# Kernel tuning notes

Measured on AMD Instinct MI355X. Metric: run time of the kernel, lower is better.

The kernel has to match this reference:

```python
import jax, jax.numpy as jnp
import numpy as np

B, S, D, H = 2, 2048, 1024, 16
DH = D // H

def setup_inputs() -> dict:
    key = jax.random.key(0)
    k1, k2, k3, k4 = jax.random.split(key, 4)
    x = jax.random.normal(k1, (B, S, D), dtype=jnp.float32)
    # flax Dense kernels: [in_features, out_features]
    w_qkv = jax.random.normal(k2, (D, 3 * D), dtype=jnp.float32) / np.sqrt(D)
    w_out = jax.random.normal(k3, (D, D), dtype=jnp.float32) / np.sqrt(D)
    b_out = jax.random.normal(k4, (D,), dtype=jnp.float32) * 0.01
    return {"x": x, "w_qkv": w_qkv, "w_out": w_out, "b_out": b_out}

def reference(x, w_qkv, w_out, b_out):
    b, s, d = x.shape
    h, dh = H, d // H
    qkv = jnp.einsum('bsd,de->bse', x, w_qkv)           # [B,S,3D]
    qkv = qkv.reshape(b, s, 3, h, dh)
    qkv = jnp.transpose(qkv, (2, 0, 3, 1, 4))            # [3,B,H,S,DH]
    q, k, v = qkv[0], qkv[1], qkv[2]
    attn = jnp.einsum('bhqd,bhkd->bhqk', q, k) / jnp.sqrt(jnp.float32(dh))
    attn = jax.nn.softmax(attn, axis=-1)                 # [B,H,S,S]
    y = jnp.einsum('bhqk,bhkd->bhqd', attn, v)           # [B,H,S,DH]
    y = jnp.transpose(y, (0, 2, 1, 3)).reshape(b, s, d)  # [B,S,D]
    return jnp.einsum('bsd,de->bse', y, w_out) + b_out
```

## Files before the change

kernel.cpp:

```cpp
#include <hip/hip_runtime.h>
#include <stdint.h>

typedef __bf16 bf16_t;
typedef __bf16 bf16x8 __attribute__((ext_vector_type(8)));
typedef float f32x4 __attribute__((ext_vector_type(4)));
typedef float f32x16 __attribute__((ext_vector_type(16)));
typedef unsigned short u16;
typedef unsigned short u16x8 __attribute__((ext_vector_type(8)));
typedef unsigned int u32;
typedef unsigned int u32x4 __attribute__((ext_vector_type(4)));

#define DEVI __device__ __forceinline__


DEVI u16 bits(float f) { bf16_t h = (bf16_t)f; return __builtin_bit_cast(u16, h); }

DEVI void gld16(const void* g, void* l) {
  __builtin_amdgcn_global_load_lds(
      (const __attribute__((address_space(1))) unsigned int*)g,
      (__attribute__((address_space(3))) unsigned int*)l, 16, 0, 0);
}

DEVI bf16x8 ldsr(const u16* s, int row, int cg) {
  const int byte = row * 128 + ((cg ^ (row & 7)) << 4);
  return *(const bf16x8*)((const char*)s + byte);
}

DEVI bf16x8 ldsrV(const u16* s, int row, int cg) {
  const int byte = row * 256 + ((cg ^ (row & 15)) << 4);
  return *(const bf16x8*)((const char*)s + byte);
}

DEVI float exp2v(float x) { return __builtin_amdgcn_exp2f(x); }

DEVI u32 cvtpk(float lo, float hi) {
  u32 r;
  asm("v_cvt_pk_bf16_f32 %0, %1, %2" : "=v"(r) : "v"(lo), "v"(hi));
  return r;
}

#define MFMA16(a, b, c) __builtin_amdgcn_mfma_f32_16x16x32_bf16(a, b, c, 0, 0, 0)
#define MFMA32(a, b, c) __builtin_amdgcn_mfma_f32_32x32x16_bf16(a, b, c, 0, 0, 0)

#define MKFRAG(dst, S, B)                                              \
  {                                                                    \
    u32 a_ = cvtpk(S[(B) + 0], S[(B) + 1]);                            \
    u32 b_ = cvtpk(S[(B) + 4], S[(B) + 5]);                            \
    u32 c_ = cvtpk(S[(B) + 2], S[(B) + 3]);                            \
    u32 d_ = cvtpk(S[(B) + 6], S[(B) + 7]);                            \
    asm("v_permlane32_swap_b32 %0, %1" : "+v"(a_), "+v"(b_));          \
    asm("v_permlane32_swap_b32 %0, %1" : "+v"(c_), "+v"(d_));          \
    u32x4 u_ = {a_, c_, b_, d_};                                       \
    dst = __builtin_bit_cast(bf16x8, u_);                              \
  }

__global__ void __launch_bounds__(256) cvt8(const float* __restrict__ in,
                                            u16* __restrict__ out, int n8) {
  const int i = blockIdx.x * 256 + threadIdx.x;
  if (i >= n8) return;
  const f32x4* p = (const f32x4*)in;
  const f32x4 a = p[2 * i], b = p[2 * i + 1];
  u16x8 o;
#pragma unroll
  for (int j = 0; j < 4; ++j) { o[j] = bits(a[j]); o[4 + j] = bits(b[j]); }
  *(u16x8*)(out + (size_t)i * 8) = o;
}

__global__ void __launch_bounds__(256) tconv(const float* __restrict__ in,
                                             u16* __restrict__ out, int K, int N) {
  __shared__ float T[64][65];
  const int k0 = blockIdx.x * 64, n0 = blockIdx.y * 64;
  const int tid = threadIdx.x;
#pragma unroll
  for (int i = 0; i < 4; ++i) {
    const int c = i * 256 + tid;
    const int row = c >> 4, c4 = c & 15;
    const f32x4 v = *(const f32x4*)(in + (size_t)(k0 + row) * N + n0 + c4 * 4);
#pragma unroll
    for (int j = 0; j < 4; ++j) T[row][c4 * 4 + j] = v[j];
  }
  __syncthreads();
#pragma unroll
  for (int i = 0; i < 2; ++i) {
    const int c = i * 256 + tid;
    const int nrow = c >> 3, k8 = c & 7;
    u16x8 o;
#pragma unroll
    for (int j = 0; j < 8; ++j) o[j] = bits(T[k8 * 8 + j][nrow]);
    *(u16x8*)(out + (size_t)(n0 + nrow) * K + k0 + k8 * 8) = o;
  }
}

__global__ void __launch_bounds__(256) vtrans(const u16* __restrict__ Vrm,
                                              u16* __restrict__ Vt) {
  __shared__ u16 T[64][72];
  const int s0 = blockIdx.x * 64;
  const int bh = blockIdx.y;
  const int tid = threadIdx.x;
#pragma unroll
  for (int i = 0; i < 2; ++i) {
    const int c = i * 256 + tid, srow = c >> 3, c8 = c & 7;
    const u16x8 v = *(const u16x8*)(Vrm + ((size_t)bh * 2048 + s0 + srow) * 64 + c8 * 8);
#pragma unroll
    for (int j = 0; j < 8; ++j) T[srow][c8 * 8 + j] = v[j];
  }
  __syncthreads();
#pragma unroll
  for (int i = 0; i < 2; ++i) {
    const int c = i * 256 + tid, dr = c >> 3, s8 = c & 7;
    u16x8 o;
#pragma unroll
    for (int j = 0; j < 8; ++j) o[j] = T[s8 * 8 + j][dr];
    *(u16x8*)(Vt + ((size_t)bh * 64 + dr) * 2048 + s0 + s8 * 8) = o;
  }
}

template <int BN>
DEVI void gemm_core(const u16* __restrict__ A, const u16* __restrict__ Bt,
                    u16* As, u16* Bs, int m0, int n0, int Kdim,
                    f32x4 (&acc)[4][BN / 32]) {
  const int NF = BN / 32;
  const int tid = threadIdx.x;
  const int l = tid & 63, w = tid >> 6;
  const int lr = l & 15, lh = l >> 4;
  const int wr = w >> 1, wc = w & 1;
  for (int kt = 0; kt < Kdim; kt += 64) {
#pragma unroll
    for (int i = 0; i < 4; ++i) {
      const int cb = i * 256 + w * 64;
      const int c = cb + l;
      const int row = c >> 3;
      const int col = ((c & 7) ^ (row & 7)) << 3;
      gld16(A + (size_t)(m0 + row) * Kdim + kt + col, As + (size_t)cb * 8);
    }
#pragma unroll
    for (int i = 0; i < BN / 32; ++i) {
      const int cb = i * 256 + w * 64;
      const int c = cb + l;
      const int row = c >> 3;
      const int col = ((c & 7) ^ (row & 7)) << 3;
      gld16(Bt + (size_t)(n0 + row) * Kdim + kt + col, Bs + (size_t)cb * 8);
    }
    __syncthreads();
#pragma unroll
    for (int kk = 0; kk < 2; ++kk) {
      bf16x8 af[4], bfr[NF];
#pragma unroll
      for (int m = 0; m < 4; ++m) af[m] = ldsr(As, wr * 64 + m * 16 + lr, kk * 4 + lh);
#pragma unroll
      for (int n = 0; n < NF; ++n)
        bfr[n] = ldsr(Bs, wc * (BN / 2) + n * 16 + lr, kk * 4 + lh);
#pragma unroll
      for (int m = 0; m < 4; ++m)
#pragma unroll
        for (int n = 0; n < NF; ++n)
          acc[m][n] = MFMA16(af[m], bfr[n], acc[m][n]);
    }
    __syncthreads();
  }
}

__global__ void __launch_bounds__(256) gemm_qkv_k(const u16* __restrict__ A,
                                                  const u16* __restrict__ Bt,
                                                  u16* __restrict__ Qb,
                                                  u16* __restrict__ Kb,
                                                  u16* __restrict__ Vb) {
  __shared__ u16 As[128 * 64], Bs[128 * 64];
  const int m0 = blockIdx.y * 128, n0 = blockIdx.x * 128;
  f32x4 acc[4][4] = {};
  gemm_core<128>(A, Bt, As, Bs, m0, n0, 1024, acc);
  const int tid = threadIdx.x;
  const int l = tid & 63, w = tid >> 6;
  const int lr = l & 15, lh = l >> 4;
  const int wr = w >> 1, wc = w & 1;
#pragma unroll
  for (int n = 0; n < 4; ++n) {
    const int ng = n0 + wc * 64 + n * 16 + lr;
    const int sel = ng >> 10, h = (ng >> 6) & 15, dh = ng & 63;
    u16* dst = sel == 0 ? Qb : (sel == 1 ? Kb : Vb);
    const float qs = (sel == 0) ? 0.125f * 1.44269504f : 1.0f;
#pragma unroll
    for (int m = 0; m < 4; ++m) {
#pragma unroll
      for (int r = 0; r < 4; ++r) {
        const int mg = m0 + wr * 64 + m * 16 + lh * 4 + r;
        const int b = mg >> 11, s = mg & 2047;
        dst[((size_t)(b * 16 + h) * 2048 + s) * 64 + dh] = bits(acc[m][n][r] * qs);
      }
    }
  }
}

__global__ void __launch_bounds__(256) gemm_out_k(const u16* __restrict__ A,
                                                  const u16* __restrict__ Bt,
                                                  const float* __restrict__ bias,
                                                  float* __restrict__ out) {
  __shared__ u16 As[128 * 64], Bs[64 * 64];
  const int m0 = blockIdx.y * 128, n0 = blockIdx.x * 64;
  f32x4 acc[4][2] = {};
  gemm_core<64>(A, Bt, As, Bs, m0, n0, 1024, acc);
  const int tid = threadIdx.x;
  const int l = tid & 63, w = tid >> 6;
  const int lr = l & 15, lh = l >> 4;
  const int wr = w >> 1, wc = w & 1;
#pragma unroll
  for (int n = 0; n < 2; ++n) {
    const int ng = n0 + wc * 32 + n * 16 + lr;
    const float bv = bias[ng];
#pragma unroll
    for (int m = 0; m < 4; ++m) {
#pragma unroll
      for (int r = 0; r < 4; ++r) {
        const int mg = m0 + wr * 64 + m * 16 + lh * 4 + r;
        out[(size_t)mg * 1024 + ng] = acc[m][n][r] + bv;
      }
    }
  }
}

__global__ void __launch_bounds__(512, 4) attn_k(const u16* __restrict__ Qb,
                                                 const u16* __restrict__ Kb,
                                                 const u16* __restrict__ Vt,
                                                 u16* __restrict__ Yb) {
  __shared__ char smem[65536];
  u16* const KsA = (u16*)smem;
  u16* const KsB = (u16*)(smem + 16384);
  u16* const VsA = (u16*)(smem + 32768);
  u16* const VsB = (u16*)(smem + 49152);

  const int tid = threadIdx.x;
  const int l = tid & 63, w = tid >> 6;
  const int lq = l & 31, hi = l >> 5;
  const int qw = w & 3;
  const int khalf = w >> 2;
  const int i0 = blockIdx.x;
  const int bid = (i0 & 7) * 64 + (i0 >> 3);
  const int bh = bid >> 4, qt = bid & 15;

  const u16* Qp = Qb + ((size_t)bh * 2048 + qt * 128 + qw * 32 + lq) * 64;
  bf16x8 qf0 = *(const bf16x8*)(Qp + hi * 8);
  bf16x8 qf1 = *(const bf16x8*)(Qp + 16 + hi * 8);
  bf16x8 qf2 = *(const bf16x8*)(Qp + 32 + hi * 8);
  bf16x8 qf3 = *(const bf16x8*)(Qp + 48 + hi * 8);

  const u16* Kbase = Kb + (size_t)bh * 2048 * 64;
  const u16* Vbase = Vt + (size_t)bh * 64 * 2048;

  bf16x8 ones;
#pragma unroll
  for (int j = 0; j < 8; ++j) ones[j] = (bf16_t)1.0f;

  f32x16 acc0 = {}, acc1 = {};
  f32x16 accs = {};

#define STAGE(Ksb, Vsb, kv0)                                               \
  {                                                                        \
    _Pragma("unroll") for (int ii = 0; ii < 2; ++ii) {                     \
      const int cb = ii * 512 + w * 64;                                    \
      const int c = cb + l;                                                \
      const int krow = c >> 3;                                             \
      const int kcol = ((c & 7) ^ (krow & 7)) << 3;                        \
      gld16(Kbase + (size_t)((kv0) + krow) * 64 + kcol, (Ksb) + cb * 8);   \
      const int vrow = c >> 4;                                             \
      const int vcol = ((c & 15) ^ (vrow & 15)) << 3;                      \
      gld16(Vbase + (size_t)vrow * 2048 + (kv0) + vcol, (Vsb) + cb * 8);   \
    }                                                                      \
  }

  STAGE(KsA, VsA, 0);
  __syncthreads();
  int cur = 0;

  for (int t = 0; t < 16; ++t) {
    u16* const Ksn = cur ? KsA : KsB;
    u16* const Vsn = cur ? VsA : VsB;
    if (t + 1 < 16) STAGE(Ksn, Vsn, (t + 1) * 128);
    const u16* Ksc = cur ? KsB : KsA;
    const u16* Vsc = cur ? VsB : VsA;

    f32x16 s0 = {}, s1 = {};
    __builtin_amdgcn_s_setprio(1);
#pragma unroll
    for (int ks = 0; ks < 4; ++ks) {
      const bf16x8 qk = ks == 0 ? qf0 : (ks == 1 ? qf1 : (ks == 2 ? qf2 : qf3));
      s0 = MFMA32(ldsr(Ksc, khalf * 64 + lq, ks * 2 + hi), qk, s0);
      s1 = MFMA32(ldsr(Ksc, khalf * 64 + 32 + lq, ks * 2 + hi), qk, s1);
    }
    __builtin_amdgcn_s_setprio(0);

#pragma unroll
    for (int i = 0; i < 16; ++i) { s0[i] = exp2v(s0[i]); s1[i] = exp2v(s1[i]); }

    bf16x8 pa0, pa1, pa2, pa3;
    MKFRAG(pa0, s0, 0);
    MKFRAG(pa1, s0, 8);
    MKFRAG(pa2, s1, 0);
    MKFRAG(pa3, s1, 8);
    __builtin_amdgcn_s_setprio(1);
    accs = MFMA32(pa0, ones, accs);
    acc0 = MFMA32(pa0, ldsrV(Vsc, lq, khalf * 8 + hi), acc0);
    acc1 = MFMA32(pa0, ldsrV(Vsc, 32 + lq, khalf * 8 + hi), acc1);
    accs = MFMA32(pa1, ones, accs);
    acc0 = MFMA32(pa1, ldsrV(Vsc, lq, khalf * 8 + 2 + hi), acc0);
    acc1 = MFMA32(pa1, ldsrV(Vsc, 32 + lq, khalf * 8 + 2 + hi), acc1);
    accs = MFMA32(pa2, ones, accs);
    acc0 = MFMA32(pa2, ldsrV(Vsc, lq, khalf * 8 + 4 + hi), acc0);
    acc1 = MFMA32(pa2, ldsrV(Vsc, 32 + lq, khalf * 8 + 4 + hi), acc1);
    accs = MFMA32(pa3, ones, accs);
    acc0 = MFMA32(pa3, ldsrV(Vsc, lq, khalf * 8 + 6 + hi), acc0);
    acc1 = MFMA32(pa3, ldsrV(Vsc, 32 + lq, khalf * 8 + 6 + hi), acc1);
    __builtin_amdgcn_s_setprio(0);

    __syncthreads();
    cur ^= 1;
  }
#undef STAGE

  float* const F = (float*)smem;
  float* const Fp = F + (size_t)(tid & 255) * 49;
  if (khalf) {
#pragma unroll
    for (int r = 0; r < 16; ++r) {
      Fp[r] = acc0[r];
      Fp[16 + r] = acc1[r];
      Fp[32 + r] = accs[r];
    }
  }
  __syncthreads();
  if (khalf) return;
#pragma unroll
  for (int r = 0; r < 16; ++r) {
    acc0[r] += Fp[r];
    acc1[r] += Fp[16 + r];
    accs[r] += Fp[32 + r];
  }

  const int b = bh >> 4, h = bh & 15;
#pragma unroll
  for (int r = 0; r < 16; ++r) {
    const float sd = 1.0f / accs[r];
    const int row = (r & 3) + 8 * (r >> 2) + 4 * hi;
    const int sq = qt * 128 + qw * 32 + row;
    u16* yp = Yb + ((size_t)b * 2048 + sq) * 1024 + h * 64;
    yp[lq] = bits(acc0[r] * sd);
    yp[32 + lq] = bits(acc1[r] * sd);
  }
}

extern "C" void kernel_launch(void* const* d_in, const int* in_sizes, int n_in,
                              void* d_out, int out_size, void* d_ws, size_t ws_size,
                              hipStream_t stream) {
  (void)in_sizes; (void)n_in; (void)out_size; (void)ws_size;
  const float* x     = (const float*)d_in[0];
  const float* w_qkv = (const float*)d_in[1];
  const float* w_out = (const float*)d_in[2];
  const float* b_out = (const float*)d_in[3];
  float* out = (float*)d_out;

  char* ws = (char*)d_ws;
  u16* xb    = (u16*)(ws);
  u16* wqkvT = (u16*)(ws + 8388608);
  u16* woutT = (u16*)(ws + 14680064);
  u16* Qb    = (u16*)(ws + 16777216);
  u16* Kb    = (u16*)(ws + 25165824);
  u16* Vrm   = (u16*)(ws + 33554432);
  u16* Vt    = (u16*)(ws + 41943040);
  u16* Yb    = xb;

  cvt8<<<2048, 256, 0, stream>>>(x, xb, 4194304 / 8);
  tconv<<<dim3(16, 48), 256, 0, stream>>>(w_qkv, wqkvT, 1024, 3072);
  tconv<<<dim3(16, 16), 256, 0, stream>>>(w_out, woutT, 1024, 1024);
  gemm_qkv_k<<<dim3(24, 32), 256, 0, stream>>>(xb, wqkvT, Qb, Kb, Vrm);
  vtrans<<<dim3(32, 32), 256, 0, stream>>>(Vrm, Vt);
  attn_k<<<512, 512, 0, stream>>>(Qb, Kb, Vt, Yb);
  gemm_out_k<<<dim3(16, 32), 256, 0, stream>>>(Yb, woutT, b_out, out);
}
```

Measured before the change: 120.0 us.

## Rewrite QKV GEMM as 256x256 tiled, 8-wave ping-pong pipelined kernel

The QKV projection GEMM moves from 128x128 tiles with 4 waves to 256x256 tiles with 8 waves. It uses double-buffered LDS fed by direct global-to-LDS loads issued in quarter-tile stages interleaved with the MFMA phases, plus barriers and s_setprio to overlap loads with math. Block indices are remapped into a grouped order for L2 reuse. This targets memory latency and load/compute serialization in the largest GEMM. In exchange it uses much more LDS and more registers per block, and launches only 192 blocks, which may underfill the GPU.

```diff
diff --git a/kernel.cpp b/kernel.cpp
--- a/kernel.cpp
+++ b/kernel.cpp
@@ -160,19 +160,146 @@
   }
 }
 
-__global__ void __launch_bounds__(256) gemm_qkv_k(const u16* __restrict__ A,
-                                                  const u16* __restrict__ Bt,
-                                                  u16* __restrict__ Qb,
-                                                  u16* __restrict__ Kb,
-                                                  u16* __restrict__ Vb) {
-  __shared__ u16 As[128 * 64], Bs[128 * 64];
-  const int m0 = blockIdx.y * 128, n0 = blockIdx.x * 128;
-  f32x4 acc[4][4] = {};
-  gemm_core<128>(A, Bt, As, Bs, m0, n0, 1024, acc);
-  const int tid = threadIdx.x;
-  const int l = tid & 63, w = tid >> 6;
+
+DEVI void stage_half(const u16* __restrict__ G, int row0, int kt, u16* dst) {
+  const int tid = threadIdx.x;
+  const int l = tid & 63, wv = tid >> 6;
+  const u16* gp = G + (size_t)row0 * 1024 + kt;
+#pragma unroll
+  for (int i = 0; i < 2; ++i) {
+    const int cb = i * 512 + wv * 64;
+    const int c = cb + l;
+    const int rih = c >> 3;
+    const int col = ((c & 7) ^ (rih & 7)) << 3;
+    gld16(gp + (size_t)rih * 1024 + col, dst + cb * 8);
+  }
+}
+
+template <bool SA1, bool SB2, int VM>
+DEVI void qkv_tile(const u16* __restrict__ A, const u16* __restrict__ Bt,
+                   int m0, int n0, int ktA1, int ktB2,
+                   u16* Ac, u16* Bc, u16* An, f32x4 (&acc)[8][4]) {
+  const int tid = threadIdx.x;
+  const int l = tid & 63, wv = tid >> 6;
   const int lr = l & 15, lh = l >> 4;
-  const int wr = w >> 1, wc = w & 1;
+  const int wr = wv >> 2, wc = wv & 3;
+  const int ab = wr * 128, bb = wc * 64;
+  bf16x8 a0[8], a1[8], b0[4], b1[4];
+#pragma unroll
+  for (int m = 0; m < 4; ++m)
+#pragma unroll
+    for (int kk = 0; kk < 2; ++kk)
+      a0[m * 2 + kk] = ldsr(Ac, ab + m * 16 + lr, kk * 4 + lh);
+#pragma unroll
+  for (int n = 0; n < 2; ++n)
+#pragma unroll
+    for (int kk = 0; kk < 2; ++kk)
+      b0[n * 2 + kk] = ldsr(Bc, bb + n * 16 + lr, kk * 4 + lh);
+  if (SA1) stage_half(A, m0, ktA1, An);
+  __builtin_amdgcn_s_barrier();
+  asm volatile("s_waitcnt lgkmcnt(0)" ::: "memory");
+  __builtin_amdgcn_sched_barrier(0);
+  __builtin_amdgcn_s_setprio(1);
+#pragma unroll
+  for (int m = 0; m < 4; ++m)
+#pragma unroll
+    for (int n = 0; n < 2; ++n)
+#pragma unroll
+      for (int kk = 0; kk < 2; ++kk)
+        acc[m][n] = MFMA16(a0[m * 2 + kk], b0[n * 2 + kk], acc[m][n]);
+  __builtin_amdgcn_s_setprio(0);
+  __builtin_amdgcn_s_barrier();
+#pragma unroll
+  for (int n = 0; n < 2; ++n)
+#pragma unroll
+    for (int kk = 0; kk < 2; ++kk)
+      b1[n * 2 + kk] = ldsr(Bc, bb + 32 + n * 16 + lr, kk * 4 + lh);
+  if (SA1) stage_half(A, m0 + 128, ktA1, An + 8192);
+  __builtin_amdgcn_s_barrier();
+  asm volatile("s_waitcnt lgkmcnt(0)" ::: "memory");
+  __builtin_amdgcn_sched_barrier(0);
+  __builtin_amdgcn_s_setprio(1);
+#pragma unroll
+  for (int m = 0; m < 4; ++m)
+#pragma unroll
+    for (int n = 0; n < 2; ++n)
+#pragma unroll
+      for (int kk = 0; kk < 2; ++kk)
+        acc[m][2 + n] = MFMA16(a0[m * 2 + kk], b1[n * 2 + kk], acc[m][2 + n]);
+  __builtin_amdgcn_s_setprio(0);
+  __builtin_amdgcn_s_barrier();
+#pragma unroll
+  for (int m = 0; m < 4; ++m)
+#pragma unroll
+    for (int kk = 0; kk < 2; ++kk)
+      a1[m * 2 + kk] = ldsr(Ac, ab + 64 + m * 16 + lr, kk * 4 + lh);
+  if (SB2) stage_half(Bt, n0, ktB2, Bc);
+  __builtin_amdgcn_s_barrier();
+  asm volatile("s_waitcnt lgkmcnt(0)" ::: "memory");
+  __builtin_amdgcn_sched_barrier(0);
+  __builtin_amdgcn_s_setprio(1);
+#pragma unroll
+  for (int m = 0; m < 4; ++m)
+#pragma unroll
+    for (int n = 0; n < 2; ++n)
+#pragma unroll
+      for (int kk = 0; kk < 2; ++kk)
+        acc[4 + m][n] = MFMA16(a1[m * 2 + kk], b0[n * 2 + kk], acc[4 + m][n]);
+  __builtin_amdgcn_s_setprio(0);
+  __builtin_amdgcn_s_barrier();
+  if (SB2) stage_half(Bt, n0 + 128, ktB2, Bc + 8192);
+  __builtin_amdgcn_s_barrier();
+  __builtin_amdgcn_s_setprio(1);
+#pragma unroll
+  for (int m = 0; m < 4; ++m)
+#pragma unroll
+    for (int n = 0; n < 2; ++n)
+#pragma unroll
+      for (int kk = 0; kk < 2; ++kk)
+        acc[4 + m][2 + n] = MFMA16(a1[m * 2 + kk], b1[n * 2 + kk], acc[4 + m][2 + n]);
+  __builtin_amdgcn_s_setprio(0);
+  if (VM == 4) asm volatile("s_waitcnt vmcnt(4)" ::: "memory");
+  else if (VM == 0) asm volatile("s_waitcnt vmcnt(0)" ::: "memory");
+  __builtin_amdgcn_s_barrier();
+}
+
+__global__ void __launch_bounds__(512, 2) gemm_qkv_k(const u16* __restrict__ A,
+                                                     const u16* __restrict__ Bt,
+                                                     u16* __restrict__ Qb,
+                                                     u16* __restrict__ Kb,
+                                                     u16* __restrict__ Vb) {
+  __shared__ u16 LA[2][16384], LB[2][16384];
+  const int bid = blockIdx.x;
+  const int g = bid & 7, w24 = bid >> 3;
+  const int mt = (g >> 1) * 4 + (w24 & 3);
+  const int nt = (g & 1) * 6 + (w24 >> 2);
+  const int m0 = mt * 256, n0 = nt * 256;
+
+  stage_half(A, m0, 0, LA[0]);
+  stage_half(A, m0 + 128, 0, LA[0] + 8192);
+  stage_half(Bt, n0, 0, LB[0]);
+  stage_half(Bt, n0 + 128, 0, LB[0] + 8192);
+  stage_half(Bt, n0, 64, LB[1]);
+  stage_half(Bt, n0 + 128, 64, LB[1] + 8192);
+  asm volatile("s_waitcnt vmcnt(4)" ::: "memory");
+  __builtin_amdgcn_s_barrier();
+
+  f32x4 acc[8][4] = {};
+  u16 *Ac = LA[0], *Bc = LB[0], *An = LA[1], *Bn = LB[1];
+#pragma unroll 1
+  for (int t = 0; t < 14; ++t) {
+    qkv_tile<true, true, 4>(A, Bt, m0, n0, (t + 1) * 64, (t + 2) * 64, Ac, Bc, An, acc);
+    u16* tp = Ac; Ac = An; An = tp;
+    tp = Bc; Bc = Bn; Bn = tp;
+  }
+  qkv_tile<true, false, 0>(A, Bt, m0, n0, 15 * 64, 0, Ac, Bc, An, acc);
+  { u16* tp = Ac; Ac = An; An = tp; tp = Bc; Bc = Bn; Bn = tp; }
+  qkv_tile<false, false, -1>(A, Bt, m0, n0, 0, 0, Ac, Bc, An, acc);
+
+  const int tid = threadIdx.x;
+  const int l = tid & 63, wv = tid >> 6;
+  const int lr = l & 15, lh = l >> 4;
+  const int wr = wv >> 2, wc = wv & 3;
 #pragma unroll
   for (int n = 0; n < 4; ++n) {
     const int ng = n0 + wc * 64 + n * 16 + lr;
@@ -180,10 +307,10 @@
     u16* dst = sel == 0 ? Qb : (sel == 1 ? Kb : Vb);
     const float qs = (sel == 0) ? 0.125f * 1.44269504f : 1.0f;
 #pragma unroll
-    for (int m = 0; m < 4; ++m) {
+    for (int m = 0; m < 8; ++m) {
 #pragma unroll
       for (int r = 0; r < 4; ++r) {
-        const int mg = m0 + wr * 64 + m * 16 + lh * 4 + r;
+        const int mg = m0 + wr * 128 + m * 16 + lh * 4 + r;
         const int b = mg >> 11, s = mg & 2047;
         dst[((size_t)(b * 16 + h) * 2048 + s) * 64 + dh] = bits(acc[m][n][r] * qs);
       }
@@ -370,7 +497,7 @@
   cvt8<<<2048, 256, 0, stream>>>(x, xb, 4194304 / 8);
   tconv<<<dim3(16, 48), 256, 0, stream>>>(w_qkv, wqkvT, 1024, 3072);
   tconv<<<dim3(16, 16), 256, 0, stream>>>(w_out, woutT, 1024, 1024);
-  gemm_qkv_k<<<dim3(24, 32), 256, 0, stream>>>(xb, wqkvT, Qb, Kb, Vrm);
+  gemm_qkv_k<<<192, 512, 0, stream>>>(xb, wqkvT, Qb, Kb, Vrm);
   vtrans<<<dim3(32, 32), 256, 0, stream>>>(Vrm, Vt);
   attn_k<<<512, 512, 0, stream>>>(Qb, Kb, Vt, Yb);
   gemm_out_k<<<dim3(16, 32), 256, 0, stream>>>(Yb, woutT, b_out, out);
```

After: 112.7 us. 6.1% less time.
